# Kernel tuning notes

Hardware: AMD Instinct MI355X
Metric: run time of the kernel (lower is better)

Reference implementation:

```python
import jax, jax.numpy as jnp
import numpy as np

B, N, OBS, HID, H = 8, 1024, 64, 192, 3
D = HID // H  # head_dim = 64
ALPHA = 0.2   # LeakyReLU negative slope
NEG = -9e15   # mask value from torch code (-9000000000000000.0)


def gat_layer(h, adj, W, a):
    """Multi-head GAT layer, math-identical to the torch per-head loop.
    h: (B,N,F_in), adj: (N,N), W: (H,F_in,D), a: (H,2D).
    Concat-score a^T [Wh_i || Wh_j] is split into a_l^T Wh_i + a_r^T Wh_j
    (broadcast-add) to avoid materializing the N^2 x 2D tensor.
    """
    Wh = jnp.einsum('bni,hid->bhnd', h, W)           # (B,H,N,D)
    d = Wh.shape[-1]
    s_i = jnp.einsum('bhnd,hd->bhn', Wh, a[:, :d])   # a_l . Wh_i
    s_j = jnp.einsum('bhnd,hd->bhn', Wh, a[:, d:])   # a_r . Wh_j
    e = s_i[..., :, None] + s_j[..., None, :]        # (B,H,N,N)
    e = jnp.where(e > 0, e, ALPHA * e)               # LeakyReLU
    e = jnp.where(adj > 0, e, NEG)                   # adjacency mask
    attn = jax.nn.softmax(e, axis=-1)                # (dropout=0 in eval)
    out = jnp.einsum('bhnm,bhmd->bhnd', attn, Wh)    # weighted aggregate
    b, nh, n, _ = out.shape
    return out.transpose(0, 2, 1, 3).reshape(b, n, nh * d)  # concat heads


def setup_inputs() -> dict:
    key = jax.random.key(0)
    k1, k2, k3, k4, k5 = jax.random.split(key, 5)
    h = jax.random.normal(k1, (B, N, OBS), dtype=jnp.float32)
    adj = jnp.ones((N, N), dtype=jnp.float32)  # graph_type='full'
    # xavier_uniform-style scale (gain=1.414)
    def xav(k, shape, fan_in, fan_out):
        lim = 1.414 * np.sqrt(6.0 / (fan_in + fan_out))
        return jax.random.uniform(k, shape, jnp.float32, -lim, lim)
    W1 = xav(k2, (H, OBS, D), OBS, D)
    a1 = xav(k3, (H, 2 * D), 2 * D, 1)
    W2 = xav(k4, (H, HID, D), HID, D)
    a2 = xav(k5, (H, 2 * D), 2 * D, 1)
    return {"h": h, "adj": adj, "W1": W1, "a1": a1, "W2": W2, "a2": a2}


def reference(h, adj, W1, a1, W2, a2):
    x = gat_layer(h, adj, W1, a1)   # (B,N,HID)
    x = jax.nn.elu(x)               # inter-layer nonlinearity
    x = gat_layer(x, adj, W2, a2)   # (B,N,HID)
    return x
```

## Files before the change

### kernel.cpp

```cpp
#include <hip/hip_runtime.h>
#include <math.h>

#define Bc   8
#define Nc   1024
#define OBSc 64
#define HIDc 192
#define NHc  3
#define Dc   64
#define ALPHAc 0.2f

typedef __attribute__((ext_vector_type(8))) _Float16 half8;
typedef __attribute__((ext_vector_type(4))) float floatx4;


__global__ __launch_bounds__(256) void k_proj1(
    const float* __restrict__ xin, const float* __restrict__ W1,
    const float* __restrict__ a1, _Float16* __restrict__ WhT,
    float* __restrict__ si, float* __restrict__ sj, float* __restrict__ Mp1,
    const float* __restrict__ adj, unsigned long long* __restrict__ adjb,
    const float* __restrict__ W2, _Float16* __restrict__ W2T)
{
    const int tid = threadIdx.x;
    const int bh  = blockIdx.y;

    if (bh == Bc * NHc) {
        const int px = blockIdx.x, wv = tid >> 6, lane = tid & 63;
        for (int r8 = 0; r8 < 8; ++r8) {
            const int i = px * 32 + wv * 8 + r8;
            unsigned long long word = 0;
            for (int g = 0; g < 16; ++g) {
                bool c = adj[(size_t)i * Nc + g * 64 + lane] > 0.f;
                unsigned long long bal = __ballot(c);
                if (lane == g) word = bal;
            }
            if (lane < 16) adjb[(size_t)i * 16 + lane] = word;
        }
        if (px < 12) {
            for (int e = px * 3072 + tid; e < px * 3072 + 3072; e += 256) {
                int t = e & 7, ln = (e >> 3) & 63, p = (e >> 9) & 1, nh = (e >> 10) & 1;
                int g = e >> 11; int ks = g % 6, hh = g / 6;
                int k = ks * 32 + (ln >> 4) * 8 + t;
                int d = nh * 32 + p * 16 + (ln & 15);
                W2T[e] = (_Float16)W2[((size_t)hh * HIDc + k) * Dc + d];
            }
        }
        return;
    }

    __shared__ union {
        _Float16 Bs[64][OBSc + 8];
        _Float16 Ts[64][40];
    } u;
    __shared__ float spsAi[32], spsAj[32], spsBi[32], spsBj[32];

    const int b = bh / NHc, hh = bh % NHc;
    const int row0 = blockIdx.x * 32;

    for (int e = tid; e < OBSc * 64; e += 256) {
        int k = e >> 6, d = e & 63;
        u.Bs[d][k] = (_Float16)W1[(size_t)hh * OBSc * 64 + e];
    }
    __syncthreads();

    const int lane = tid & 63, wv = tid >> 6;
    const int mblk = (wv & 1) * 16, nhalf = (wv >> 1) * 32;
    const int fr = lane & 15, fq = lane >> 4;
    floatx4 acc0 = {0.f,0.f,0.f,0.f}, acc1 = {0.f,0.f,0.f,0.f};
    const int row = row0 + mblk + fr;

#pragma unroll
    for (int ks = 0; ks < OBSc / 32; ++ks) {
        const int k0 = ks * 32 + fq * 8;
        const float* xr = xin + ((size_t)b * Nc + row) * OBSc + k0;
        float4 u0 = *(const float4*)xr;
        float4 u1 = *(const float4*)(xr + 4);
        half8 af;
        af[0] = (_Float16)u0.x; af[1] = (_Float16)u0.y;
        af[2] = (_Float16)u0.z; af[3] = (_Float16)u0.w;
        af[4] = (_Float16)u1.x; af[5] = (_Float16)u1.y;
        af[6] = (_Float16)u1.z; af[7] = (_Float16)u1.w;
        half8 b0 = *(const half8*)&u.Bs[nhalf + fr][k0];
        half8 b1 = *(const half8*)&u.Bs[nhalf + 16 + fr][k0];
        acc0 = __builtin_amdgcn_mfma_f32_16x16x32_f16(af, b0, acc0, 0, 0, 0);
        acc1 = __builtin_amdgcn_mfma_f32_16x16x32_f16(af, b1, acc1, 0, 0, 0);
    }

    const float al0 = a1[hh * 2 * Dc + nhalf + fr];
    const float al1 = a1[hh * 2 * Dc + nhalf + 16 + fr];
    const float ar0 = a1[hh * 2 * Dc + Dc + nhalf + fr];
    const float ar1 = a1[hh * 2 * Dc + Dc + nhalf + 16 + fr];
    float pi[4], pj[4];
#pragma unroll
    for (int r = 0; r < 4; ++r) {
        pi[r] = acc0[r] * al0 + acc1[r] * al1;
        pj[r] = acc0[r] * ar0 + acc1[r] * ar1;
        for (int off = 8; off >= 1; off >>= 1) {
            pi[r] += __shfl_xor(pi[r], off, 64);
            pj[r] += __shfl_xor(pj[r], off, 64);
        }
    }
    if (fr == 0) {
#pragma unroll
        for (int r = 0; r < 4; ++r) {
            int lr = mblk + fq * 4 + r;
            if (nhalf == 0) { spsAi[lr] = pi[r]; spsAj[lr] = pj[r]; }
            else            { spsBi[lr] = pi[r]; spsBj[lr] = pj[r]; }
        }
    }
    __syncthreads();
    if (tid < 64) {
        float vj = -INFINITY;
        if (tid < 32) {
            size_t g = (size_t)bh * Nc + row0 + tid;
            si[g] = spsAi[tid] + spsBi[tid];
            vj    = spsAj[tid] + spsBj[tid];
            sj[g] = vj;
        }
        float mv = vj;
        for (int off = 32; off >= 1; off >>= 1) mv = fmaxf(mv, __shfl_xor(mv, off, 64));
        if (tid == 0) Mp1[bh * 32 + blockIdx.x] = mv;
    }

#pragma unroll
    for (int nt = 0; nt < 2; ++nt) {
        const int d = nhalf + nt * 16 + fr;
        floatx4 acc = nt ? acc1 : acc0;
#pragma unroll
        for (int p = 0; p < 2; ++p) {
            union { unsigned int w; _Float16 h[2]; } pk;
            pk.h[0] = (_Float16)acc[2 * p];
            pk.h[1] = (_Float16)acc[2 * p + 1];
            *(unsigned int*)&u.Ts[d][mblk + fq * 4 + 2 * p] = pk.w;
        }
    }
    __syncthreads();
    {
        const int c2 = tid >> 6, lane2 = tid & 63;
        const int fr2 = lane2 & 15, fq2 = lane2 >> 4;
        const int jt = row0 >> 5;
        uint4 v = *(const uint4*)&u.Ts[c2 * 16 + fr2][fq2 * 8];
        *(uint4*)&WhT[(size_t)(bh * 32 + jt) * 2048 + tid * 8] = v;
    }
}

__global__ __launch_bounds__(384, 2) void k_fused(
    const _Float16* __restrict__ WhT1,
    const float* __restrict__ si1, const float* __restrict__ sj1,
    const float* __restrict__ Mp1, const unsigned long long* __restrict__ adjb,
    const _Float16* __restrict__ W2T, const float* __restrict__ a2,
    _Float16* __restrict__ WhT2,
    float* __restrict__ si2, float* __restrict__ sj2, float* __restrict__ Mp2)
{
    __shared__ union {
        struct { float red[6][64][20]; float zs[6][16]; } ag;
        _Float16 Ts3[3][64][24];
    } uR;
    __shared__ _Float16 xhs[16][208];
    __shared__ float sp2i[6][16], sp2j[6][16];
    __shared__ float sjs[3][1024];
    __shared__ unsigned long long adjs[16][16];

    const int tid = threadIdx.x, wv = tid >> 6, lane = tid & 63;
    const int b = blockIdx.x & 7, c16 = blockIdx.x >> 3;
    const int row0 = c16 * 16;
    const int hh = wv >> 1, kh = wv & 1;
    const int bh = b * NHc + hh;
    const int fr = lane & 15, fq = lane >> 4;
    const int row = row0 + fr;

    for (int e = tid; e < 768; e += 384) {
        int h = e >> 8, idx = (e & 255) * 4;
        *(float4*)&sjs[h][idx] = *(const float4*)&sj1[(size_t)(b * NHc + h) * Nc + idx];
    }
    if (tid < 256)
        adjs[tid >> 4][tid & 15] = adjb[(size_t)(row0 + (tid >> 4)) * 16 + (tid & 15)];
    __syncthreads();

    float mpv = Mp1[bh * 32 + (lane & 31)];
    for (int off = 16; off >= 1; off >>= 1) mpv = fmaxf(mpv, __shfl_xor(mpv, off, 64));
    const float s_i = si1[(size_t)bh * Nc + row];
    const float em  = s_i + mpv;
    const float m_i = fmaxf(em, ALPHAc * em);

    const _Float16* Bp = WhT1 + (size_t)bh * 65536 + (size_t)kh * 32768 + lane * 8;

    floatx4 acc[4] = {{0.f,0.f,0.f,0.f},{0.f,0.f,0.f,0.f},
                      {0.f,0.f,0.f,0.f},{0.f,0.f,0.f,0.f}};
    float zacc = 0.f;

    half8 bf[3][4];
#pragma unroll
    for (int st = 0; st < 2; ++st)
#pragma unroll
        for (int c = 0; c < 4; ++c)
            bf[st][c] = *(const half8*)(Bp + (size_t)st * 2048 + c * 512);

#pragma unroll
    for (int s16 = 0; s16 < 16; ++s16) {
        const int s   = kh * 16 + s16;
        const int cur = s16 % 3;
        if (s16 < 14) {
            const int nxt = (s16 + 2) % 3;
            const _Float16* bn = Bp + (size_t)(s16 + 2) * 2048;
#pragma unroll
            for (int c = 0; c < 4; ++c)
                bf[nxt][c] = *(const half8*)(bn + c * 512);
        }
        const float4 sa = *(const float4*)&sjs[hh][s * 32 + fq * 8];
        const float4 sb = *(const float4*)&sjs[hh][s * 32 + fq * 8 + 4];
        const unsigned long long w = adjs[fr][s >> 1];
        const int bb = (s & 1) * 32 + fq * 8;
        const float sv[8] = {sa.x, sa.y, sa.z, sa.w, sb.x, sb.y, sb.z, sb.w};
        float p[8];
        if (w == ~0ULL) {
#pragma unroll
            for (int t = 0; t < 8; ++t) {
                float e = s_i + sv[t];
                e = fmaxf(e, ALPHAc * e) - m_i;
                p[t] = __expf(e);
            }
        } else {
#pragma unroll
            for (int t = 0; t < 8; ++t) {
                float e = s_i + sv[t];
                e = fmaxf(e, ALPHAc * e) - m_i;
                e = ((w >> (bb + t)) & 1) ? e : -1e30f;
                p[t] = __expf(e);
            }
        }
        zacc += ((p[0] + p[1]) + (p[2] + p[3])) + ((p[4] + p[5]) + (p[6] + p[7]));
        union { half8 v; _Float16 h[8]; } A;
#pragma unroll
        for (int t = 0; t < 8; ++t) A.h[t] = (_Float16)p[t];
        acc[0] = __builtin_amdgcn_mfma_f32_16x16x32_f16(A.v, bf[cur][0], acc[0], 0, 0, 0);
        acc[1] = __builtin_amdgcn_mfma_f32_16x16x32_f16(A.v, bf[cur][1], acc[1], 0, 0, 0);
        acc[2] = __builtin_amdgcn_mfma_f32_16x16x32_f16(A.v, bf[cur][2], acc[2], 0, 0, 0);
        acc[3] = __builtin_amdgcn_mfma_f32_16x16x32_f16(A.v, bf[cur][3], acc[3], 0, 0, 0);
    }

    zacc += __shfl_xor(zacc, 16, 64);
    zacc += __shfl_xor(zacc, 32, 64);
    if (lane < 16) uR.ag.zs[wv][lane] = zacc;
#pragma unroll
    for (int c = 0; c < 4; ++c)
        *(floatx4*)&uR.ag.red[wv][lane][c * 4] = acc[c];
    __syncthreads();

    {
        const int w0 = hh * 2;
#pragma unroll
        for (int cc = 0; cc < 2; ++cc) {
            const int c = kh * 2 + cc;
#pragma unroll
            for (int reg = 0; reg < 4; ++reg) {
                const int r = fq * 4 + reg;
                const float af = uR.ag.red[w0][lane][c * 4 + reg]
                               + uR.ag.red[w0 + 1][lane][c * 4 + reg];
                const float Z = uR.ag.zs[w0][r] + uR.ag.zs[w0 + 1][r];
                float v = af / Z;
                v = v > 0.f ? v : expm1f(v);
                xhs[r][hh * 64 + c * 16 + fr] = (_Float16)v;
            }
        }
    }
    __syncthreads();

    floatx4 a2c0 = {0.f,0.f,0.f,0.f}, a2c1 = {0.f,0.f,0.f,0.f};
#pragma unroll
    for (int ks = 0; ks < 6; ++ks) {
        half8 af2 = *(const half8*)&xhs[fr][ks * 32 + fq * 8];
        const _Float16* wb = W2T + (size_t)((hh * 6 + ks) * 2 + kh) * 1024 + lane * 8;
        half8 b0 = *(const half8*)wb;
        half8 b1 = *(const half8*)(wb + 512);
        a2c0 = __builtin_amdgcn_mfma_f32_16x16x32_f16(af2, b0, a2c0, 0, 0, 0);
        a2c1 = __builtin_amdgcn_mfma_f32_16x16x32_f16(af2, b1, a2c1, 0, 0, 0);
    }

    {
        const float* a2h = a2 + hh * 2 * Dc;
        const float al0 = a2h[kh * 32 + fr];
        const float al1 = a2h[kh * 32 + 16 + fr];
        const float ar0 = a2h[Dc + kh * 32 + fr];
        const float ar1 = a2h[Dc + kh * 32 + 16 + fr];
#pragma unroll
        for (int reg = 0; reg < 4; ++reg) {
            float pi = a2c0[reg] * al0 + a2c1[reg] * al1;
            float pj = a2c0[reg] * ar0 + a2c1[reg] * ar1;
            for (int off = 8; off >= 1; off >>= 1) {
                pi += __shfl_xor(pi, off, 64);
                pj += __shfl_xor(pj, off, 64);
            }
            if (fr == 0) {
                sp2i[wv][fq * 4 + reg] = pi;
                sp2j[wv][fq * 4 + reg] = pj;
            }
        }
    }
    __syncthreads();

    if (kh == 0 && lane < 16) {
        const int r = lane;
        float vi = sp2i[wv][r] + sp2i[wv + 1][r];
        float vj = sp2j[wv][r] + sp2j[wv + 1][r];
        si2[(size_t)bh * Nc + row0 + r] = vi;
        sj2[(size_t)bh * Nc + row0 + r] = vj;
        float mv = vj;
        for (int off = 8; off >= 1; off >>= 1) mv = fmaxf(mv, __shfl_xor(mv, off, 64));
        if (r == 0) Mp2[bh * 64 + c16] = mv;
    }
#pragma unroll
    for (int cc = 0; cc < 2; ++cc) {
        const int d = kh * 32 + cc * 16 + fr;
        floatx4 av = cc ? a2c1 : a2c0;
#pragma unroll
        for (int p = 0; p < 2; ++p) {
            union { unsigned int w2; _Float16 h[2]; } pk;
            pk.h[0] = (_Float16)av[2 * p];
            pk.h[1] = (_Float16)av[2 * p + 1];
            *(unsigned int*)&uR.Ts3[hh][d][fq * 4 + 2 * p] = pk.w2;
        }
    }
    __syncthreads();

    {
        const int hh3 = tid / 128, rem = tid % 128, d3 = rem >> 1, rr = rem & 1;
        uint4 v = *(const uint4*)&uR.Ts3[hh3][d3][rr * 8];
        const int bh3 = b * NHc + hh3;
        const int jt = c16 >> 1;
        const int c3 = d3 >> 4;
        const int fqp = (c16 & 1) * 2 + rr;
        *(uint4*)&WhT2[((((size_t)(bh3 * 32 + jt) * 4 + c3) * 64) + fqp * 16 + (d3 & 15)) * 8] = v;
    }
}

__global__ __launch_bounds__(256, 4) void k_aggr2(
    const _Float16* __restrict__ WhT,
    const float* __restrict__ si, const float* __restrict__ sj,
    const float* __restrict__ Mp2, const unsigned long long* __restrict__ adjb,
    float* __restrict__ out)
{
    __shared__ float red[4][64][20];
    __shared__ float zs[4][16];
    __shared__ float sjs[1024];
    __shared__ unsigned long long adjs[16][16];

    const int tid  = threadIdx.x;
    const int wv   = tid >> 6, lane = tid & 63;
    const int bh   = blockIdx.x % 24;
    const int row0 = (blockIdx.x / 24) << 4;
    const int b    = bh / NHc, hh = bh % NHc;
    const int fr   = lane & 15, fq = lane >> 4;
    const int row  = row0 + fr;

    *(float4*)&sjs[tid * 4] = *(const float4*)&sj[(size_t)bh * Nc + tid * 4];
    if (tid < 256)
        adjs[tid >> 4][tid & 15] = adjb[(size_t)(row0 + (tid >> 4)) * 16 + (tid & 15)];
    __syncthreads();

    float mpv = Mp2[bh * 64 + lane];
    for (int off = 32; off >= 1; off >>= 1) mpv = fmaxf(mpv, __shfl_xor(mpv, off, 64));

    const float s_i = si[(size_t)bh * Nc + row];
    const float em  = s_i + mpv;
    const float m_i = fmaxf(em, ALPHAc * em);

    const _Float16* Bp = WhT + (size_t)bh * 65536 + (size_t)wv * 8 * 2048 + lane * 8;

    floatx4 acc[4] = {{0.f,0.f,0.f,0.f},{0.f,0.f,0.f,0.f},
                      {0.f,0.f,0.f,0.f},{0.f,0.f,0.f,0.f}};
    float zacc = 0.f;

    half8 bf[3][4];
#pragma unroll
    for (int st = 0; st < 2; ++st)
#pragma unroll
        for (int c = 0; c < 4; ++c)
            bf[st][c] = *(const half8*)(Bp + (size_t)st * 2048 + c * 512);

#pragma unroll
    for (int s8 = 0; s8 < 8; ++s8) {
        const int s   = wv * 8 + s8;
        const int cur = s8 % 3;
        if (s8 < 6) {
            const int nxt = (s8 + 2) % 3;
            const _Float16* bn = Bp + (size_t)(s8 + 2) * 2048;
#pragma unroll
            for (int c = 0; c < 4; ++c)
                bf[nxt][c] = *(const half8*)(bn + c * 512);
        }
        const float4 sa = *(const float4*)&sjs[s * 32 + fq * 8];
        const float4 sb = *(const float4*)&sjs[s * 32 + fq * 8 + 4];
        const unsigned long long w = adjs[fr][s >> 1];
        const int bb = (s & 1) * 32 + fq * 8;
        const float sv[8] = {sa.x, sa.y, sa.z, sa.w, sb.x, sb.y, sb.z, sb.w};
        float p[8];
        if (w == ~0ULL) {
#pragma unroll
            for (int t = 0; t < 8; ++t) {
                float e = s_i + sv[t];
                e = fmaxf(e, ALPHAc * e) - m_i;
                p[t] = __expf(e);
            }
        } else {
#pragma unroll
            for (int t = 0; t < 8; ++t) {
                float e = s_i + sv[t];
                e = fmaxf(e, ALPHAc * e) - m_i;
                e = ((w >> (bb + t)) & 1) ? e : -1e30f;
                p[t] = __expf(e);
            }
        }
        zacc += ((p[0] + p[1]) + (p[2] + p[3])) + ((p[4] + p[5]) + (p[6] + p[7]));
        union { half8 v; _Float16 h[8]; } A;
#pragma unroll
        for (int t = 0; t < 8; ++t) A.h[t] = (_Float16)p[t];
        acc[0] = __builtin_amdgcn_mfma_f32_16x16x32_f16(A.v, bf[cur][0], acc[0], 0, 0, 0);
        acc[1] = __builtin_amdgcn_mfma_f32_16x16x32_f16(A.v, bf[cur][1], acc[1], 0, 0, 0);
        acc[2] = __builtin_amdgcn_mfma_f32_16x16x32_f16(A.v, bf[cur][2], acc[2], 0, 0, 0);
        acc[3] = __builtin_amdgcn_mfma_f32_16x16x32_f16(A.v, bf[cur][3], acc[3], 0, 0, 0);
    }

    zacc += __shfl_xor(zacc, 16, 64);
    zacc += __shfl_xor(zacc, 32, 64);
    if (lane < 16) zs[wv][lane] = zacc;
#pragma unroll
    for (int c = 0; c < 4; ++c)
        *(floatx4*)&red[wv][lane][c * 4] = acc[c];
    __syncthreads();

    floatx4 af = {0.f, 0.f, 0.f, 0.f};
#pragma unroll
    for (int w2 = 0; w2 < 4; ++w2) {
        floatx4 r = *(const floatx4*)&red[w2][lane][wv * 4];
        af[0] += r[0]; af[1] += r[1]; af[2] += r[2]; af[3] += r[3];
    }
#pragma unroll
    for (int reg = 0; reg < 4; ++reg) {
        const int r = fq * 4 + reg;
        const float Z = (zs[0][r] + zs[1][r]) + (zs[2][r] + zs[3][r]);
        out[((size_t)b * Nc + row0 + r) * HIDc + hh * Dc + wv * 16 + fr] = af[reg] / Z;
    }
}

extern "C" void kernel_launch(void* const* d_in, const int* in_sizes, int n_in,
                              void* d_out, int out_size, void* d_ws, size_t ws_size,
                              hipStream_t stream) {
    const float* h_in = (const float*)d_in[0];
    const float* adj  = (const float*)d_in[1];
    const float* W1   = (const float*)d_in[2];
    const float* a1   = (const float*)d_in[3];
    const float* W2   = (const float*)d_in[4];
    const float* a2   = (const float*)d_in[5];
    float* out = (float*)d_out;

    float* ws = (float*)d_ws;
    const size_t nWhT_f = (size_t)Bc * NHc * Dc * Nc / 2;
    const size_t nAb_f  = (size_t)Nc * 16 * 2;
    const size_t nW2T_f = 36864 / 2;
    const size_t nR     = (size_t)Bc * NHc * Nc;
    _Float16* WhT1 = (_Float16*)ws;
    _Float16* WhT2 = (_Float16*)(ws + nWhT_f);
    unsigned long long* adjb = (unsigned long long*)(ws + 2 * nWhT_f);
    _Float16* W2T  = (_Float16*)(ws + 2 * nWhT_f + nAb_f);
    float* si1 = ws + 2 * nWhT_f + nAb_f + nW2T_f;
    float* sj1 = si1 + nR;
    float* si2 = sj1 + nR;
    float* sj2 = si2 + nR;
    float* Mp1 = sj2 + nR;
    float* Mp2 = Mp1 + 768;

    k_proj1<<<dim3(Nc / 32, Bc * NHc + 1), 256, 0, stream>>>(
        h_in, W1, a1, WhT1, si1, sj1, Mp1, adj, adjb, W2, W2T);

    k_fused<<<512, 384, 0, stream>>>(
        WhT1, si1, sj1, Mp1, adjb, W2T, a2, WhT2, si2, sj2, Mp2);

    k_aggr2<<<1536, 256, 0, stream>>>(WhT2, si2, sj2, Mp2, adjb, out);
}
```

Before: 118.6 us.

## Process two 16-row tiles per block in k_aggr2 to reuse WhT loads

k_aggr2 now handles 32 query rows per block (two M-tiles) instead of 16. Each B fragment loaded from WhT2 therefore feeds two MFMAs, which halves global WhT traffic and the grid size. The cost is doubled accumulator registers, larger shared memory, and a lower occupancy bound. The block index in k_fused is also remapped so that consecutive blocks share the same batch, which may improve cache locality.

Result: slower. 128.0 us (+8.0%).

```diff
diff --git a/kernel.cpp b/kernel.cpp
--- a/kernel.cpp
+++ b/kernel.cpp
@@ -161,7 +161,7 @@
     __shared__ unsigned long long adjs[16][16];
 
     const int tid = threadIdx.x, wv = tid >> 6, lane = tid & 63;
-    const int b = blockIdx.x & 7, c16 = blockIdx.x >> 3;
+    const int b = blockIdx.x >> 6, c16 = blockIdx.x & 63;
     const int row0 = c16 * 16;
     const int hh = wv >> 1, kh = wv & 1;
     const int bh = b * NHc + hh;
@@ -333,42 +333,45 @@
     }
 }
 
-__global__ __launch_bounds__(256, 4) void k_aggr2(
+__global__ __launch_bounds__(256, 3) void k_aggr2(
     const _Float16* __restrict__ WhT,
     const float* __restrict__ si, const float* __restrict__ sj,
     const float* __restrict__ Mp2, const unsigned long long* __restrict__ adjb,
     float* __restrict__ out)
 {
-    __shared__ float red[4][64][20];
-    __shared__ float zs[4][16];
+    __shared__ float red[4][64][33];
+    __shared__ float zs[4][2][16];
     __shared__ float sjs[1024];
-    __shared__ unsigned long long adjs[16][16];
+    __shared__ unsigned long long adjs[32][16];
 
     const int tid  = threadIdx.x;
     const int wv   = tid >> 6, lane = tid & 63;
-    const int bh   = blockIdx.x % 24;
-    const int row0 = (blockIdx.x / 24) << 4;
+    const int bh   = blockIdx.x >> 5;
+    const int row0 = (blockIdx.x & 31) << 5;
     const int b    = bh / NHc, hh = bh % NHc;
     const int fr   = lane & 15, fq = lane >> 4;
-    const int row  = row0 + fr;
 
     *(float4*)&sjs[tid * 4] = *(const float4*)&sj[(size_t)bh * Nc + tid * 4];
-    if (tid < 256)
-        adjs[tid >> 4][tid & 15] = adjb[(size_t)(row0 + (tid >> 4)) * 16 + (tid & 15)];
+    for (int e = tid; e < 512; e += 256)
+        adjs[e >> 4][e & 15] = adjb[(size_t)(row0 + (e >> 4)) * 16 + (e & 15)];
     __syncthreads();
 
     float mpv = Mp2[bh * 64 + lane];
     for (int off = 32; off >= 1; off >>= 1) mpv = fmaxf(mpv, __shfl_xor(mpv, off, 64));
 
-    const float s_i = si[(size_t)bh * Nc + row];
-    const float em  = s_i + mpv;
-    const float m_i = fmaxf(em, ALPHAc * em);
+    float s_i[2], m_i[2];
+#pragma unroll
+    for (int mt = 0; mt < 2; ++mt) {
+        s_i[mt] = si[(size_t)bh * Nc + row0 + mt * 16 + fr];
+        const float em = s_i[mt] + mpv;
+        m_i[mt] = fmaxf(em, ALPHAc * em);
+    }
 
     const _Float16* Bp = WhT + (size_t)bh * 65536 + (size_t)wv * 8 * 2048 + lane * 8;
 
-    floatx4 acc[4] = {{0.f,0.f,0.f,0.f},{0.f,0.f,0.f,0.f},
-                      {0.f,0.f,0.f,0.f},{0.f,0.f,0.f,0.f}};
-    float zacc = 0.f;
+    floatx4 acc[2][4] = {{{0.f,0.f,0.f,0.f},{0.f,0.f,0.f,0.f},{0.f,0.f,0.f,0.f},{0.f,0.f,0.f,0.f}},
+                         {{0.f,0.f,0.f,0.f},{0.f,0.f,0.f,0.f},{0.f,0.f,0.f,0.f},{0.f,0.f,0.f,0.f}}};
+    float zacc[2] = {0.f, 0.f};
 
     half8 bf[3][4];
 #pragma unroll
@@ -390,55 +393,68 @@
         }
         const float4 sa = *(const float4*)&sjs[s * 32 + fq * 8];
         const float4 sb = *(const float4*)&sjs[s * 32 + fq * 8 + 4];
-        const unsigned long long w = adjs[fr][s >> 1];
         const int bb = (s & 1) * 32 + fq * 8;
         const float sv[8] = {sa.x, sa.y, sa.z, sa.w, sb.x, sb.y, sb.z, sb.w};
-        float p[8];
-        if (w == ~0ULL) {
-#pragma unroll
-            for (int t = 0; t < 8; ++t) {
-                float e = s_i + sv[t];
-                e = fmaxf(e, ALPHAc * e) - m_i;
-                p[t] = __expf(e);
-            }
-        } else {
-#pragma unroll
-            for (int t = 0; t < 8; ++t) {
-                float e = s_i + sv[t];
-                e = fmaxf(e, ALPHAc * e) - m_i;
-                e = ((w >> (bb + t)) & 1) ? e : -1e30f;
-                p[t] = __expf(e);
-            }
-        }
-        zacc += ((p[0] + p[1]) + (p[2] + p[3])) + ((p[4] + p[5]) + (p[6] + p[7]));
-        union { half8 v; _Float16 h[8]; } A;
-#pragma unroll
-        for (int t = 0; t < 8; ++t) A.h[t] = (_Float16)p[t];
-        acc[0] = __builtin_amdgcn_mfma_f32_16x16x32_f16(A.v, bf[cur][0], acc[0], 0, 0, 0);
-        acc[1] = __builtin_amdgcn_mfma_f32_16x16x32_f16(A.v, bf[cur][1], acc[1], 0, 0, 0);
-        acc[2] = __builtin_amdgcn_mfma_f32_16x16x32_f16(A.v, bf[cur][2], acc[2], 0, 0, 0);
-        acc[3] = __builtin_amdgcn_mfma_f32_16x16x32_f16(A.v, bf[cur][3], acc[3], 0, 0, 0);
-    }
-
-    zacc += __shfl_xor(zacc, 16, 64);
-    zacc += __shfl_xor(zacc, 32, 64);
-    if (lane < 16) zs[wv][lane] = zacc;
-#pragma unroll
-    for (int c = 0; c < 4; ++c)
-        *(floatx4*)&red[wv][lane][c * 4] = acc[c];
-    __syncthreads();
-
-    floatx4 af = {0.f, 0.f, 0.f, 0.f};
-#pragma unroll
-    for (int w2 = 0; w2 < 4; ++w2) {
-        floatx4 r = *(const floatx4*)&red[w2][lane][wv * 4];
-        af[0] += r[0]; af[1] += r[1]; af[2] += r[2]; af[3] += r[3];
-    }
-#pragma unroll
-    for (int reg = 0; reg < 4; ++reg) {
-        const int r = fq * 4 + reg;
-        const float Z = (zs[0][r] + zs[1][r]) + (zs[2][r] + zs[3][r]);
-        out[((size_t)b * Nc + row0 + r) * HIDc + hh * Dc + wv * 16 + fr] = af[reg] / Z;
+        half8 Av[2];
+#pragma unroll
+        for (int mt = 0; mt < 2; ++mt) {
+            const unsigned long long w = adjs[mt * 16 + fr][s >> 1];
+            float p[8];
+            if (w == ~0ULL) {
+#pragma unroll
+                for (int t = 0; t < 8; ++t) {
+                    float e = s_i[mt] + sv[t];
+                    e = fmaxf(e, ALPHAc * e) - m_i[mt];
+                    p[t] = __expf(e);
+                }
+            } else {
+#pragma unroll
+                for (int t = 0; t < 8; ++t) {
+                    float e = s_i[mt] + sv[t];
+                    e = fmaxf(e, ALPHAc * e) - m_i[mt];
+                    e = ((w >> (bb + t)) & 1) ? e : -1e30f;
+                    p[t] = __expf(e);
+                }
+            }
+            zacc[mt] += ((p[0]+p[1]) + (p[2]+p[3])) + ((p[4]+p[5]) + (p[6]+p[7]));
+            union { half8 v; _Float16 h[8]; } A;
+#pragma unroll
+            for (int t = 0; t < 8; ++t) A.h[t] = (_Float16)p[t];
+            Av[mt] = A.v;
+        }
+#pragma unroll
+        for (int c = 0; c < 4; ++c) {
+            acc[0][c] = __builtin_amdgcn_mfma_f32_16x16x32_f16(Av[0], bf[cur][c], acc[0][c], 0, 0, 0);
+            acc[1][c] = __builtin_amdgcn_mfma_f32_16x16x32_f16(Av[1], bf[cur][c], acc[1][c], 0, 0, 0);
+        }
+    }
+
+#pragma unroll
+    for (int mt = 0; mt < 2; ++mt) {
+        zacc[mt] += __shfl_xor(zacc[mt], 16, 64);
+        zacc[mt] += __shfl_xor(zacc[mt], 32, 64);
+        if (lane < 16) zs[wv][mt][lane] = zacc[mt];
+#pragma unroll
+        for (int c = 0; c < 4; ++c)
+            *(floatx4*)&red[wv][lane][mt * 16 + c * 4] = acc[mt][c];
+    }
+    __syncthreads();
+
+#pragma unroll
+    for (int mt = 0; mt < 2; ++mt) {
+        floatx4 af = {0.f, 0.f, 0.f, 0.f};
+#pragma unroll
+        for (int w2 = 0; w2 < 4; ++w2) {
+            floatx4 r = *(const floatx4*)&red[w2][lane][mt * 16 + wv * 4];
+            af[0] += r[0]; af[1] += r[1]; af[2] += r[2]; af[3] += r[3];
+        }
+#pragma unroll
+        for (int reg = 0; reg < 4; ++reg) {
+            const int r = fq * 4 + reg;
+            const float Z = (zs[0][mt][r] + zs[1][mt][r]) + (zs[2][mt][r] + zs[3][mt][r]);
+            out[((size_t)b * Nc + row0 + mt * 16 + r) * HIDc + hh * Dc + wv * 16 + fr]
+                = af[reg] / Z;
+        }
     }
 }
 
@@ -475,5 +491,5 @@
     k_fused<<<512, 384, 0, stream>>>(
         WhT1, si1, sj1, Mp1, adjb, W2T, a2, WhT2, si2, sj2, Mp2);
 
-    k_aggr2<<<1536, 256, 0, stream>>>(WhT2, si2, sj2, Mp2, adjb, out);
+    k_aggr2<<<768, 256, 0, stream>>>(WhT2, si2, sj2, Mp2, adjb, out);
 }
```
